# Performance work log

Measured on AMD Instinct MI355X. Metric: run time of the kernel, lower is better.

The kernel has to match this reference:

```python
import jax, jax.numpy as jnp
import numpy as np

B, N1, N2, D, K = 8, 2048, 512, 128, 32
LEVELS, RES, BASE, FC = 3, 3, 0.25, 192
R3 = RES ** 3  # 27 voxel bins per level
EPS = 1e-5


def group_norm(x, gamma, beta, groups):
    # x: [b, C, ...]; normalize per (group) over channel-subset + spatial dims
    b, c = x.shape[0], x.shape[1]
    xg = x.reshape(b, groups, -1)
    mu = xg.mean(axis=-1, keepdims=True)
    var = xg.var(axis=-1, keepdims=True)
    xn = ((xg - mu) * jax.lax.rsqrt(var + EPS)).reshape(x.shape)
    shape = (1, c) + (1,) * (x.ndim - 2)
    return xn * gamma.reshape(shape) + beta.reshape(shape)


def prelu(x, a):
    return jnp.where(x >= 0, x, a * x)


def setup_inputs() -> dict:
    key = jax.random.key(0)
    ks = jax.random.split(key, 12)
    def w(k, shape):
        fan_in = shape[-1]
        return jax.random.uniform(k, shape, jnp.float32, -1.0, 1.0) / jnp.sqrt(jnp.float32(fan_in))
    return {
        "coords": jax.random.normal(ks[0], (B, N1, 3), jnp.float32),
        "coords2": jax.random.normal(ks[1], (B, N2, 3), jnp.float32),
        "fmap1": jax.random.normal(ks[2], (B, D, N1), jnp.float32),
        "fmap2": jax.random.normal(ks[3], (B, D, N2), jnp.float32),
        # vol_conv: Conv1d(81,128,1) -> GN(8,128) -> PReLU -> Conv1d(128,192,1)
        "W1": w(ks[4], (128, R3 * LEVELS)), "b1": jnp.zeros((128,), jnp.float32),
        "g1": jnp.ones((128,), jnp.float32), "be1": jnp.zeros((128,), jnp.float32),
        "a1": jnp.array(0.25, jnp.float32),
        "W2": w(ks[5], (FC, 128)), "b2": jnp.zeros((FC,), jnp.float32),
        # knn_conv: Conv2d(4,64,1) -> GN(8,64) -> PReLU;  knn_out: Conv1d(64,192,1)
        "Wk": w(ks[6], (64, 4)), "bk": jnp.zeros((64,), jnp.float32),
        "gk": jnp.ones((64,), jnp.float32), "bek": jnp.zeros((64,), jnp.float32),
        "ak": jnp.array(0.25, jnp.float32),
        "Wo": w(ks[7], (FC, 64)), "bo": jnp.zeros((FC,), jnp.float32),
    }


def reference(coords, coords2, fmap1, fmap2, W1, b1, g1, be1, a1, W2, b2,
              Wk, bk, gk, bek, ak, Wo, bo):
    b, n1 = coords.shape[0], coords.shape[1]
    n2 = coords2.shape[1]
    dim = fmap1.shape[1]

    # correlation: [b, n1, n2]
    corr = jnp.einsum('bdn,bdm->bnm', fmap1, fmap2) / jnp.sqrt(jnp.float32(dim))
    # pairwise offsets template - search: [b, n1, n2, 3]
    diff = coords2[:, None, :, :] - coords[:, :, None, :]

    # --- multi-level voxel feature via scatter-add ---
    base = jnp.arange(b * n1, dtype=jnp.int32).reshape(b, n1, 1) * R3
    feats = []
    for i in range(LEVELS):
        r = BASE * (2 ** i)
        dv = jnp.round(diff / r)
        valid = jnp.all(jnp.abs(dv) <= (RES // 2), axis=-1)          # [b,n1,n2]
        dvi = (dv + 1.0).astype(jnp.int32)
        cube = dvi[..., 0] * (RES * RES) + dvi[..., 1] * RES + dvi[..., 2]
        idx = jnp.where(valid, cube, 0)                              # torch: cube*valid
        seg = (base + idx).reshape(-1)
        vf = valid.astype(corr.dtype)
        nseg = b * n1 * R3
        add = jax.ops.segment_sum((corr * vf).reshape(-1), seg, num_segments=nseg).reshape(b, n1, R3)
        cnt = jax.ops.segment_sum(vf.reshape(-1), seg, num_segments=nseg).reshape(b, n1, R3)
        feats.append((add / jnp.clip(cnt, 1.0, float(n1))).transpose(0, 2, 1))  # [b,R3,n1]
    vol = jnp.concatenate(feats, axis=1)                             # [b, 3*27, n1]

    h = jnp.einsum('oc,bcn->bon', W1, vol) + b1[None, :, None]
    h = prelu(group_norm(h, g1, be1, 8), a1)
    vol_out = jnp.einsum('oc,bcn->bon', W2, h) + b2[None, :, None]   # [b, FC, n1]

    # --- KNN feature ---
    dist = jnp.sum(diff * diff, axis=-1)                             # [b,n1,n2]
    _, nbr = jax.lax.top_k(-dist, K)                                 # [b,n1,K]
    knn_corr = jnp.take_along_axis(corr, nbr, axis=2)                # [b,n1,K]
    knn_xyz = jnp.take_along_axis(diff, nbr[..., None], axis=2)      # [b,n1,K,3]
    e = jnp.concatenate([knn_corr[:, None], knn_xyz.transpose(0, 3, 1, 2)], axis=1)  # [b,4,n1,K]
    h = jnp.einsum('oc,bcnk->bonk', Wk, e) + bk[None, :, None, None]
    h = prelu(group_norm(h, gk, bek, 8), ak)
    h = jnp.max(h, axis=3)                                           # [b,64,n1]
    knn_out = jnp.einsum('oc,bcn->bon', Wo, h) + bo[None, :, None]   # [b,FC,n1]

    return vol_out + knn_out
```

## Files before the change

### kernel.cpp

```cpp
#include <hip/hip_runtime.h>
#include <hip/hip_bf16.h>

#define N1 2048
#define N2 512
#define KNN 32

typedef unsigned short u16;
typedef unsigned int u32;
typedef unsigned long long u64;
typedef __attribute__((ext_vector_type(8))) short bf16x8;
typedef __attribute__((ext_vector_type(4))) float f32x4;

#define OFF_W1B  18432
#define OFF_GV   36864
#define OFF_GK   36992
#define OFF_FLAG 37120
#define OFF_H1   37128
#define OFF_KM   1085704
#define OFF_CO   1609992

__device__ __forceinline__ float tof(u16 u) {
  union { u32 i; float f; } v; v.i = ((u32)u) << 16; return v.f;
}
__device__ __forceinline__ u16 tob(float f) {
  __hip_bfloat16 h = __float2bfloat16(f);
  return *reinterpret_cast<u16*>(&h);
}
__device__ __forceinline__ float fs(float v) {
  return (fabsf(v) < 1e30f) ? v : 0.f;
}

template <int BF>
__device__ __forceinline__ float LD(const void* p, size_t i) {
  if (BF) return tof(((const u16*)p)[i]);
  return ((const float*)p)[i];
}
template <int BF>
__device__ __forceinline__ void ST(void* p, size_t i, float v) {
  if (BF) ((u16*)p)[i] = tob(v);
  else    ((float*)p)[i] = v;
}

__device__ __forceinline__ u32 umin32(u32 a, u32 b) { return a < b ? a : b; }

__device__ __forceinline__ u32 wave_min_u32(u32 v) {
  v = umin32(v, (u32)__builtin_amdgcn_update_dpp((int)0xFFFFFFFF, (int)v, 0x111, 0xf, 0xf, false));
  v = umin32(v, (u32)__builtin_amdgcn_update_dpp((int)0xFFFFFFFF, (int)v, 0x112, 0xf, 0xf, false));
  v = umin32(v, (u32)__builtin_amdgcn_update_dpp((int)0xFFFFFFFF, (int)v, 0x114, 0xf, 0xf, false));
  v = umin32(v, (u32)__builtin_amdgcn_update_dpp((int)0xFFFFFFFF, (int)v, 0x118, 0xf, 0xf, false));
  v = umin32(v, (u32)__builtin_amdgcn_update_dpp((int)0xFFFFFFFF, (int)v, 0x142, 0xa, 0xf, false));
  v = umin32(v, (u32)__builtin_amdgcn_update_dpp((int)0xFFFFFFFF, (int)v, 0x143, 0xc, 0xf, false));
  return (u32)__builtin_amdgcn_readlane((int)v, 63);
}

template <int BF>
__device__ __forceinline__ bf16x8 ld_wfrag(const void* W2, const void* Wo,
                                           int o, int k0) {
  if (BF) {
    const u16* p = (k0 < 128) ? (const u16*)W2 + (size_t)o * 128 + k0
                              : (const u16*)Wo + (size_t)o * 64 + (k0 - 128);
    return *(const bf16x8*)p;
  } else {
    const float* p = (k0 < 128) ? (const float*)W2 + (size_t)o * 128 + k0
                                : (const float*)Wo + (size_t)o * 64 + (k0 - 128);
    bf16x8 r;
#pragma unroll
    for (int j = 0; j < 8; j++) r[j] = (short)tob(p[j]);
    return r;
  }
}

template <int BF>
__device__ void prep_body(const void* W1, float* ws, int i0, int stride) {
  u16* w1b = (u16*)(ws + OFF_W1B);
  for (int i = i0; i < 128 * 96; i += stride) {
    int c = i / 96, j = i % 96;
    float v = (j < 81) ? LD<BF>(W1, c * 81 + j) : 0.f;
    w1b[i] = tob(fs(v));
  }
}

__global__ __launch_bounds__(256) void k_prep(const void* fmap1, const void* W1,
                                              float* ws) {
  int t = threadIdx.x;
  __shared__ int sbad;
  if (t == 0) sbad = 0;
  __syncthreads();
  int bad = 0;
  const u16* fm = (const u16*)fmap1;
  for (int i = t * 8; i < t * 8 + 8; i++) {
    float v = tof(fm[i]);
    if (!(fabsf(v) <= 64.f)) bad = 1;
  }
  if (bad) atomicOr(&sbad, 1);
  __syncthreads();
  int bf = sbad ? 0 : 1;
  if (blockIdx.x == 0) {
    if (t == 0) ((int*)(ws + OFF_FLAG))[0] = bf;
    (ws + OFF_GV)[t] = 0.f;
  }
  int i0 = blockIdx.x * 256 + t, stride = gridDim.x * 256;
  if (bf) prep_body<1>(W1, ws, i0, stride);
  else    prep_body<0>(W1, ws, i0, stride);
}

template <int BF>
__device__ void corr_stage(const void* f1, const void* f2, u16* As, u16* Bs,
                           int b, int m0, int n0, int t) {
#pragma unroll
  for (int rep = 0; rep < 2; rep++) {
    int i = t + rep * 256;
    int m8 = i & 15, d4 = i >> 4;
    u16 e[4][8];
    if (BF) {
      const u16* F1 = (const u16*)f1;
#pragma unroll
      for (int dr = 0; dr < 4; dr++) {
        uint4 v = *(const uint4*)&F1[(size_t)(b * 128 + d4 * 4 + dr) * N1 + m0 + m8 * 8];
        u32 w[4] = {v.x, v.y, v.z, v.w};
#pragma unroll
        for (int j = 0; j < 8; j++) e[dr][j] = (u16)(w[j >> 1] >> ((j & 1) * 16));
      }
    } else {
      const float* F1 = (const float*)f1;
#pragma unroll
      for (int dr = 0; dr < 4; dr++) {
        const float* src = &F1[(size_t)(b * 128 + d4 * 4 + dr) * N1 + m0 + m8 * 8];
        float4 a = *(const float4*)src, c = *(const float4*)(src + 4);
        float f[8] = {a.x, a.y, a.z, a.w, c.x, c.y, c.z, c.w};
#pragma unroll
        for (int j = 0; j < 8; j++) e[dr][j] = tob(f[j]);
      }
    }
#pragma unroll
    for (int j = 0; j < 8; j++) {
      u64 pk = (u64)e[0][j] | ((u64)e[1][j] << 16) | ((u64)e[2][j] << 32) |
               ((u64)e[3][j] << 48);
      *(u64*)&As[(m8 * 8 + j) * 136 + d4 * 4] = pk;
    }
  }
  {
    int n8 = t & 7, d4 = t >> 3;
    u16 e[4][8];
    if (BF) {
      const u16* F2 = (const u16*)f2;
#pragma unroll
      for (int dr = 0; dr < 4; dr++) {
        uint4 v = *(const uint4*)&F2[(size_t)(b * 128 + d4 * 4 + dr) * N2 + n0 + n8 * 8];
        u32 w[4] = {v.x, v.y, v.z, v.w};
#pragma unroll
        for (int j = 0; j < 8; j++) e[dr][j] = (u16)(w[j >> 1] >> ((j & 1) * 16));
      }
    } else {
      const float* F2 = (const float*)f2;
#pragma unroll
      for (int dr = 0; dr < 4; dr++) {
        const float* src = &F2[(size_t)(b * 128 + d4 * 4 + dr) * N2 + n0 + n8 * 8];
        float4 a = *(const float4*)src, c = *(const float4*)(src + 4);
        float f[8] = {a.x, a.y, a.z, a.w, c.x, c.y, c.z, c.w};
#pragma unroll
        for (int j = 0; j < 8; j++) e[dr][j] = tob(f[j]);
      }
    }
#pragma unroll
    for (int j = 0; j < 8; j++) {
      u64 pk = (u64)e[0][j] | ((u64)e[1][j] << 16) | ((u64)e[2][j] << 32) |
               ((u64)e[3][j] << 48);
      *(u64*)&Bs[(n8 * 8 + j) * 136 + d4 * 4] = pk;
    }
  }
}

__global__ __launch_bounds__(256) void k_corr(const int* flag,
                                              const void* f1, const void* f2,
                                              u16* corrb) {
  __shared__ __attribute__((aligned(16))) u16 As[128 * 136];
  __shared__ __attribute__((aligned(16))) u16 Bs[64 * 136];
  int b = blockIdx.z, m0 = blockIdx.x * 128, n0 = blockIdx.y * 64, t = threadIdx.x;
  if (*flag) corr_stage<1>(f1, f2, As, Bs, b, m0, n0, t);
  else       corr_stage<0>(f1, f2, As, Bs, b, m0, n0, t);
  __syncthreads();

  int wv = t >> 6, lane = t & 63;
  int l15 = lane & 15, q = lane >> 4;
  int wm = (wv >> 1) * 64, wn = (wv & 1) * 32;
  f32x4 acc[4][2];
#pragma unroll
  for (int mt = 0; mt < 4; mt++)
#pragma unroll
    for (int nt = 0; nt < 2; nt++) acc[mt][nt] = (f32x4){0.f, 0.f, 0.f, 0.f};

#pragma unroll
  for (int kc = 0; kc < 128; kc += 32) {
    bf16x8 af[4], bf[2];
#pragma unroll
    for (int mt = 0; mt < 4; mt++)
      af[mt] = *(const bf16x8*)&As[(wm + mt * 16 + l15) * 136 + kc + q * 8];
#pragma unroll
    for (int nt = 0; nt < 2; nt++)
      bf[nt] = *(const bf16x8*)&Bs[(wn + nt * 16 + l15) * 136 + kc + q * 8];
#pragma unroll
    for (int mt = 0; mt < 4; mt++)
#pragma unroll
      for (int nt = 0; nt < 2; nt++)
        acc[mt][nt] = __builtin_amdgcn_mfma_f32_16x16x32_bf16(
            af[mt], bf[nt], acc[mt][nt], 0, 0, 0);
  }
  const float s = 0.08838834764831843f;
#pragma unroll
  for (int mt = 0; mt < 4; mt++)
#pragma unroll
    for (int nt = 0; nt < 2; nt++)
#pragma unroll
      for (int r = 0; r < 4; r++) {
        int m = m0 + wm + mt * 16 + q * 4 + r;
        int n = n0 + wn + nt * 16 + l15;
        corrb[((size_t)(b * N1 + m)) * N2 + n] = tob(acc[mt][nt][r] * s);
      }
}

template <int BF>
__device__ void pv_body(const void* coords, const void* coords2,
                        const u16* corrb, const void* Wk, const void* bk,
                        const u16* w1b, const void* b1,
                        u16* h1b, u16* knnmax,
                        float* gvolraw, float* gknnraw,
                        float* c2s, float* binsum, float* bincnt,
                        float4* e_s, u16* volb, float* statv, float* statk,
                        int b, int p0, int t) {
  int wv = t >> 6, lane = t & 63;
  int l15 = lane & 15, q = lane >> 4;
  for (int i = t; i < N2 * 3; i += 256) c2s[i] = LD<BF>(coords2, b * N2 * 3 + i);
  for (int i = t; i < 208; i += 256) ((uint4*)volb)[i] = make_uint4(0, 0, 0, 0);
  if (t < 16) { statv[t] = 0.f; statk[t] = 0.f; }
  __syncthreads();

  for (int s = 0; s < 2; s++) {
    int pp = wv * 2 + s;
    int p = p0 + pp;
    for (int i = lane; i < 81; i += 64) {
      binsum[wv * 81 + i] = 0.f;
      bincnt[wv * 81 + i] = 0.f;
    }
    float px = LD<BF>(coords, (b * N1 + p) * 3 + 0);
    float py = LD<BF>(coords, (b * N1 + p) * 3 + 1);
    float pz = LD<BF>(coords, (b * N1 + p) * 3 + 2);
    const u16* crow = corrb + ((size_t)(b * N1 + p)) * N2;

    u64 kk[8];
#pragma unroll
    for (int i = 0; i < 8; i++) {
      int n2 = i * 64 + lane;
      float cv = tof(crow[n2]);
      float dx = c2s[n2 * 3 + 0] - px;
      float dy = c2s[n2 * 3 + 1] - py;
      float dz = c2s[n2 * 3 + 2] - pz;
      float dist = __fadd_rn(__fadd_rn(__fmul_rn(dx, dx), __fmul_rn(dy, dy)),
                             __fmul_rn(dz, dz));
      union { float f; u32 u; } du; du.f = dist;
      kk[i] = (((u64)du.u) << 32) | (u64)n2;
      float sc = 4.f;
#pragma unroll
      for (int lvl = 0; lvl < 3; lvl++) {
        float vx = rintf(dx * sc), vy = rintf(dy * sc), vz = rintf(dz * sc);
        if (fabsf(vx) <= 1.f && fabsf(vy) <= 1.f && fabsf(vz) <= 1.f) {
          int cube = ((int)vx + 1) * 9 + ((int)vy + 1) * 3 + ((int)vz + 1);
          atomicAdd(&binsum[wv * 81 + lvl * 27 + cube], cv);
          atomicAdd(&bincnt[wv * 81 + lvl * 27 + cube], 1.f);
        }
        sc *= 0.5f;
      }
    }

#define CAS(a, b) { u64 x = kk[a], y = kk[b]; bool sw = y < x; \
                    kk[a] = sw ? y : x; kk[b] = sw ? x : y; }
    CAS(0,1) CAS(2,3) CAS(4,5) CAS(6,7)
    CAS(0,2) CAS(1,3) CAS(4,6) CAS(5,7)
    CAS(1,2) CAS(5,6)
    CAS(0,4) CAS(1,5) CAS(2,6) CAS(3,7)
    CAS(2,4) CAS(3,5)
    CAS(1,2) CAS(3,4) CAS(5,6)
#undef CAS
    int my_idx = 0;
    for (int it = 0; it < KNN; it++) {
      u32 hb = (u32)(kk[0] >> 32);
      u32 wb = wave_min_u32(hb);
      u64 mask = __ballot(hb == wb);
      u32 widx;
      if (__builtin_popcountll(mask) == 1) {
        int wl = (int)__builtin_ctzll(mask);
        widx = (u32)__builtin_amdgcn_readlane((int)(u32)kk[0], wl);
      } else {
        u32 hidx = (hb == wb) ? (u32)kk[0] : 0xFFFFFFFFu;
        widx = wave_min_u32(hidx);
      }
      if (lane == it) my_idx = (int)widx;
      if (lane == (int)(widx & 63u)) {
        kk[0] = kk[1]; kk[1] = kk[2]; kk[2] = kk[3]; kk[3] = kk[4];
        kk[4] = kk[5]; kk[5] = kk[6]; kk[6] = kk[7]; kk[7] = ~0ull;
      }
    }
    if (lane < KNN) {
      float4 ev;
      ev.x = tof(crow[my_idx]);
      ev.y = c2s[my_idx * 3 + 0] - px;
      ev.z = c2s[my_idx * 3 + 1] - py;
      ev.w = c2s[my_idx * 3 + 2] - pz;
      e_s[wv * 32 + lane] = ev;
    }
#pragma unroll
    for (int rep = 0; rep < 2; rep++) {
      int i = lane + rep * 64;
      if (i < 96) {
        float v = (i < 81)
            ? binsum[wv * 81 + i] / fmaxf(bincnt[wv * 81 + i], 1.f) : 0.f;
        volb[pp * 104 + i] = tob(v);
      }
    }

    {
      int cch = lane;
      float w0 = LD<BF>(Wk, cch * 4 + 0), w1 = LD<BF>(Wk, cch * 4 + 1);
      float w2 = LD<BF>(Wk, cch * 4 + 2), w3 = LD<BF>(Wk, cch * 4 + 3);
      float bv = LD<BF>(bk, cch);
      float sm = 0.f, sq = 0.f, mx = -3e38f;
#pragma unroll 8
      for (int k = 0; k < KNN; k++) {
        float4 ev = e_s[wv * 32 + k];
        float h = bv + w0 * ev.x + w1 * ev.y + w2 * ev.z + w3 * ev.w;
        sm += h; sq += h * h; mx = fmaxf(mx, h);
      }
      knnmax[((size_t)(b * N1 + p)) * 64 + cch] = tob(mx);
      sm += __shfl_xor(sm, 1, 64); sq += __shfl_xor(sq, 1, 64);
      sm += __shfl_xor(sm, 2, 64); sq += __shfl_xor(sq, 2, 64);
      sm += __shfl_xor(sm, 4, 64); sq += __shfl_xor(sq, 4, 64);
      if ((lane & 7) == 0) {
        int g = cch >> 3;
        atomicAdd(&statk[g * 2 + 0], sm);
        atomicAdd(&statk[g * 2 + 1], sq);
      }
    }
  }
  __syncthreads();

  f32x4 acc[2];
  acc[0] = (f32x4){0.f, 0.f, 0.f, 0.f};
  acc[1] = (f32x4){0.f, 0.f, 0.f, 0.f};
#pragma unroll
  for (int kc = 0; kc < 96; kc += 32) {
    bf16x8 af = *(const bf16x8*)&volb[l15 * 104 + kc + q * 8];
    bf16x8 bf0 = *(const bf16x8*)&w1b[((2 * wv + 0) * 16 + l15) * 96 + kc + q * 8];
    bf16x8 bf1 = *(const bf16x8*)&w1b[((2 * wv + 1) * 16 + l15) * 96 + kc + q * 8];
    acc[0] = __builtin_amdgcn_mfma_f32_16x16x32_bf16(af, bf0, acc[0], 0, 0, 0);
    acc[1] = __builtin_amdgcn_mfma_f32_16x16x32_bf16(af, bf1, acc[1], 0, 0, 0);
  }
#pragma unroll
  for (int ct = 0; ct < 2; ct++) {
    int c = (2 * wv + ct) * 16 + l15;
    float bias = LD<BF>(b1, c);
    float sm = 0.f, sq = 0.f;
    if (q < 2) {
#pragma unroll
      for (int r = 0; r < 4; r++) {
        int p = p0 + q * 4 + r;
        float v = acc[ct][r] + bias;
        h1b[((size_t)(b * N1 + p)) * 128 + c] = tob(v);
        sm += v; sq += v * v;
      }
    }
    sm += __shfl_xor(sm, 1, 64);  sq += __shfl_xor(sq, 1, 64);
    sm += __shfl_xor(sm, 2, 64);  sq += __shfl_xor(sq, 2, 64);
    sm += __shfl_xor(sm, 4, 64);  sq += __shfl_xor(sq, 4, 64);
    sm += __shfl_xor(sm, 8, 64);  sq += __shfl_xor(sq, 8, 64);
    sm += __shfl_xor(sm, 16, 64); sq += __shfl_xor(sq, 16, 64);
    sm += __shfl_xor(sm, 32, 64); sq += __shfl_xor(sq, 32, 64);
    if (lane == 0) {
      int g = 2 * wv + ct;
      atomicAdd(&statv[g * 2 + 0], sm);
      atomicAdd(&statv[g * 2 + 1], sq);
    }
  }
  __syncthreads();
  if (t < 16) atomicAdd(&gvolraw[b * 16 + t], statv[t]);
  else if (t < 32) atomicAdd(&gknnraw[b * 16 + (t - 16)], statk[t - 16]);
}

__global__ __launch_bounds__(256) void k_pv(const int* flag,
                                            const void* coords, const void* coords2,
                                            const u16* corrb, const void* Wk,
                                            const void* bk, const u16* w1b,
                                            const void* b1, u16* h1b,
                                            u16* knnmax, float* gvolraw,
                                            float* gknnraw) {
  __shared__ float c2s[N2 * 3];
  __shared__ float binsum[4 * 81];
  __shared__ float bincnt[4 * 81];
  __shared__ float4 e_s[4 * 32];
  __shared__ __attribute__((aligned(16))) u16 volb[16 * 104];
  __shared__ float statv[16], statk[16];
  int b = blockIdx.y, p0 = blockIdx.x * 8, t = threadIdx.x;
  if (*flag)
    pv_body<1>(coords, coords2, corrb, Wk, bk, w1b, b1, h1b, knnmax,
               gvolraw, gknnraw, c2s, binsum, bincnt, e_s, volb, statv, statk,
               b, p0, t);
  else
    pv_body<0>(coords, coords2, corrb, Wk, bk, w1b, b1, h1b, knnmax,
               gvolraw, gknnraw, c2s, binsum, bincnt, e_s, volb, statv, statk,
               b, p0, t);
}

template <int BF>
__device__ void out_body(const u16* h1b, const u16* knnmax,
                         const void* W2, const void* Wo,
                         const float* gvolraw, const float* gknnraw,
                         const void* g1, const void* be1, const void* a1p,
                         const void* gk, const void* bek, const void* akp,
                         const void* b2, const void* bo, void* out,
                         float* Ac, float* Bc, float* Sc, float* Bi, u16* gs,
                         int b, int p0, int t) {
  if (t < 192) {
    float A, Bv, slope;
    if (t < 128) {
      int g = t >> 4;
      float S = fs(gvolraw[b * 16 + g * 2 + 0]);
      float Q = fs(gvolraw[b * 16 + g * 2 + 1]);
      float mean = S / 32768.f;
      float var = fmaxf(Q / 32768.f - mean * mean, 0.f);
      float inv = 1.f / sqrtf(var + 1e-5f);
      A = inv * LD<BF>(g1, t); Bv = LD<BF>(be1, t) - mean * A;
      slope = LD<BF>(a1p, 0);
    } else {
      int c = t - 128, g = c >> 3;
      float S = fs(gknnraw[b * 16 + g * 2 + 0]);
      float Q = fs(gknnraw[b * 16 + g * 2 + 1]);
      float mean = S / 524288.f;
      float var = fmaxf(Q / 524288.f - mean * mean, 0.f);
      float inv = 1.f / sqrtf(var + 1e-5f);
      A = inv * LD<BF>(gk, c); Bv = LD<BF>(bek, c) - mean * A;
      slope = LD<BF>(akp, 0);
    }
    Ac[t] = A; Bc[t] = Bv; Sc[t] = slope;
    Bi[t] = LD<BF>(b2, t) + LD<BF>(bo, t);
  }
  __syncthreads();

  for (int i = t; i < 768; i += 256) {
    int p = i / 24, c8 = i % 24;
    int c0 = c8 * 8;
    uint4 v;
    if (c8 < 16) v = *(const uint4*)&h1b[((size_t)(b * N1 + p0 + p)) * 128 + c0];
    else         v = *(const uint4*)&knnmax[((size_t)(b * N1 + p0 + p)) * 64 + (c0 - 128)];
    u16 e[8] = {(u16)(v.x & 0xffff), (u16)(v.x >> 16), (u16)(v.y & 0xffff),
                (u16)(v.y >> 16),    (u16)(v.z & 0xffff), (u16)(v.z >> 16),
                (u16)(v.w & 0xffff), (u16)(v.w >> 16)};
    u16 r[8];
#pragma unroll
    for (int j = 0; j < 8; j++) {
      int c = c0 + j;
      float xn = tof(e[j]) * Ac[c] + Bc[c];
      xn = xn >= 0.f ? xn : Sc[c] * xn;
      r[j] = tob(xn);
    }
    uint4 wv;
    wv.x = (u32)r[0] | ((u32)r[1] << 16);
    wv.y = (u32)r[2] | ((u32)r[3] << 16);
    wv.z = (u32)r[4] | ((u32)r[5] << 16);
    wv.w = (u32)r[6] | ((u32)r[7] << 16);
    *(uint4*)&gs[p * 200 + c0] = wv;
  }
  __syncthreads();

  int wv2 = t >> 6, lane = t & 63;
  int l15 = lane & 15, q = lane >> 4;
  int obase = wv2 * 48;
  f32x4 acc[3][2];
#pragma unroll
  for (int mt = 0; mt < 3; mt++)
#pragma unroll
    for (int nt = 0; nt < 2; nt++) acc[mt][nt] = (f32x4){0.f, 0.f, 0.f, 0.f};

#pragma unroll
  for (int kc = 0; kc < 192; kc += 32) {
    bf16x8 af[3], bf[2];
#pragma unroll
    for (int mt = 0; mt < 3; mt++)
      af[mt] = ld_wfrag<BF>(W2, Wo, obase + mt * 16 + l15, kc + q * 8);
#pragma unroll
    for (int nt = 0; nt < 2; nt++)
      bf[nt] = *(const bf16x8*)&gs[(nt * 16 + l15) * 200 + kc + q * 8];
#pragma unroll
    for (int mt = 0; mt < 3; mt++)
#pragma unroll
      for (int nt = 0; nt < 2; nt++)
        acc[mt][nt] = __builtin_amdgcn_mfma_f32_16x16x32_bf16(
            af[mt], bf[nt], acc[mt][nt], 0, 0, 0);
  }
#pragma unroll
  for (int mt = 0; mt < 3; mt++)
#pragma unroll
    for (int nt = 0; nt < 2; nt++)
#pragma unroll
      for (int r = 0; r < 4; r++) {
        int o = obase + mt * 16 + q * 4 + r;
        int p = p0 + nt * 16 + l15;
        ST<BF>(out, ((size_t)(b * 192 + o)) * N1 + p, fs(acc[mt][nt][r] + Bi[o]));
      }
}

__global__ __launch_bounds__(256) void k_out(const int* flag,
                                             const u16* h1b, const u16* knnmax,
                                             const void* W2, const void* Wo,
                                             const float* gvolraw, const float* gknnraw,
                                             const void* g1, const void* be1,
                                             const void* a1p, const void* gk,
                                             const void* bek, const void* akp,
                                             const void* b2, const void* bo,
                                             void* out) {
  __shared__ float Ac[192], Bc[192], Sc[192], Bi[192];
  __shared__ __attribute__((aligned(16))) u16 gs[32 * 200];
  int b = blockIdx.y, p0 = blockIdx.x * 32, t = threadIdx.x;
  if (*flag)
    out_body<1>(h1b, knnmax, W2, Wo, gvolraw, gknnraw, g1, be1, a1p, gk, bek,
                akp, b2, bo, out, Ac, Bc, Sc, Bi, gs, b, p0, t);
  else
    out_body<0>(h1b, knnmax, W2, Wo, gvolraw, gknnraw, g1, be1, a1p, gk, bek,
                akp, b2, bo, out, Ac, Bc, Sc, Bi, gs, b, p0, t);
}

extern "C" void kernel_launch(void* const* d_in, const int* in_sizes, int n_in,
                              void* d_out, int out_size, void* d_ws, size_t ws_size,
                              hipStream_t stream) {
  const void* coords  = d_in[0];
  const void* coords2 = d_in[1];
  const void* fmap1   = d_in[2];
  const void* fmap2   = d_in[3];
  const void* W1  = d_in[4];
  const void* b1  = d_in[5];
  const void* g1  = d_in[6];
  const void* be1 = d_in[7];
  const void* a1  = d_in[8];
  const void* W2  = d_in[9];
  const void* b2  = d_in[10];
  const void* Wk  = d_in[11];
  const void* bk  = d_in[12];
  const void* gk  = d_in[13];
  const void* bek = d_in[14];
  const void* ak  = d_in[15];
  const void* Wo  = d_in[16];
  const void* bo  = d_in[17];

  float* ws = (float*)d_ws;
  u16* w1b       = (u16*)(ws + OFF_W1B);
  float* gvolraw = ws + OFF_GV;
  float* gknnraw = ws + OFF_GK;
  const int* flag = (const int*)(ws + OFF_FLAG);
  u16* h1b    = (u16*)(ws + OFF_H1);
  u16* knnmax = (u16*)(ws + OFF_KM);
  u16* corrb  = (u16*)(ws + OFF_CO);

  k_prep<<<dim3(8), dim3(256), 0, stream>>>(fmap1, W1, ws);
  k_corr<<<dim3(16, 8, 8), dim3(256), 0, stream>>>(flag, fmap1, fmap2, corrb);
  k_pv<<<dim3(256, 8), dim3(256), 0, stream>>>(flag, coords, coords2, corrb,
                                               Wk, bk, w1b, b1, h1b, knnmax,
                                               gvolraw, gknnraw);
  k_out<<<dim3(64, 8), dim3(256), 0, stream>>>(flag, h1b, knnmax, W2, Wo,
                                               gvolraw, gknnraw, g1, be1, a1,
                                               gk, bek, ak, b2, bo, d_out);
}
```

Baseline: 208.2 us.

## Fuse correlation GEMM into per-point kernel and shrink output tile

Drops the separate correlation kernel and its global bf16 corr buffer. Each k_pv block now computes its 8 rows of corr in shared memory with MFMA, reading fmap1 columns and all of fmap2 in 64-column chunks. This removes the corr write and re-read through global memory and one launch. The cost is that every block reloads and converts the full fmap2 for its batch (256 blocks per batch), and half of each 16-row MFMA tile is padding. k_out is also retiled to 16 points per block to launch more blocks.

```diff
diff --git a/kernel.cpp b/kernel.cpp
--- a/kernel.cpp
+++ b/kernel.cpp
@@ -17,7 +17,6 @@
 #define OFF_FLAG 37120
 #define OFF_H1   37128
 #define OFF_KM   1085704
-#define OFF_CO   1609992
 
 __device__ __forceinline__ float tof(u16 u) {
   union { u32 i; float f; } v; v.i = ((u32)u) << 16; return v.f;
@@ -105,134 +104,80 @@
 }
 
 template <int BF>
-__device__ void corr_stage(const void* f1, const void* f2, u16* As, u16* Bs,
-                           int b, int m0, int n0, int t) {
-#pragma unroll
-  for (int rep = 0; rep < 2; rep++) {
-    int i = t + rep * 256;
-    int m8 = i & 15, d4 = i >> 4;
-    u16 e[4][8];
-    if (BF) {
-      const u16* F1 = (const u16*)f1;
-#pragma unroll
-      for (int dr = 0; dr < 4; dr++) {
-        uint4 v = *(const uint4*)&F1[(size_t)(b * 128 + d4 * 4 + dr) * N1 + m0 + m8 * 8];
-        u32 w[4] = {v.x, v.y, v.z, v.w};
-#pragma unroll
-        for (int j = 0; j < 8; j++) e[dr][j] = (u16)(w[j >> 1] >> ((j & 1) * 16));
-      }
-    } else {
-      const float* F1 = (const float*)f1;
-#pragma unroll
-      for (int dr = 0; dr < 4; dr++) {
-        const float* src = &F1[(size_t)(b * 128 + d4 * 4 + dr) * N1 + m0 + m8 * 8];
-        float4 a = *(const float4*)src, c = *(const float4*)(src + 4);
-        float f[8] = {a.x, a.y, a.z, a.w, c.x, c.y, c.z, c.w};
-#pragma unroll
-        for (int j = 0; j < 8; j++) e[dr][j] = tob(f[j]);
-      }
-    }
-#pragma unroll
-    for (int j = 0; j < 8; j++) {
-      u64 pk = (u64)e[0][j] | ((u64)e[1][j] << 16) | ((u64)e[2][j] << 32) |
-               ((u64)e[3][j] << 48);
-      *(u64*)&As[(m8 * 8 + j) * 136 + d4 * 4] = pk;
-    }
-  }
-  {
-    int n8 = t & 7, d4 = t >> 3;
-    u16 e[4][8];
-    if (BF) {
-      const u16* F2 = (const u16*)f2;
-#pragma unroll
-      for (int dr = 0; dr < 4; dr++) {
-        uint4 v = *(const uint4*)&F2[(size_t)(b * 128 + d4 * 4 + dr) * N2 + n0 + n8 * 8];
-        u32 w[4] = {v.x, v.y, v.z, v.w};
-#pragma unroll
-        for (int j = 0; j < 8; j++) e[dr][j] = (u16)(w[j >> 1] >> ((j & 1) * 16));
-      }
-    } else {
-      const float* F2 = (const float*)f2;
-#pragma unroll
-      for (int dr = 0; dr < 4; dr++) {
-        const float* src = &F2[(size_t)(b * 128 + d4 * 4 + dr) * N2 + n0 + n8 * 8];
-        float4 a = *(const float4*)src, c = *(const float4*)(src + 4);
-        float f[8] = {a.x, a.y, a.z, a.w, c.x, c.y, c.z, c.w};
-#pragma unroll
-        for (int j = 0; j < 8; j++) e[dr][j] = tob(f[j]);
-      }
-    }
-#pragma unroll
-    for (int j = 0; j < 8; j++) {
-      u64 pk = (u64)e[0][j] | ((u64)e[1][j] << 16) | ((u64)e[2][j] << 32) |
-               ((u64)e[3][j] << 48);
-      *(u64*)&Bs[(n8 * 8 + j) * 136 + d4 * 4] = pk;
-    }
-  }
-}
-
-__global__ __launch_bounds__(256) void k_corr(const int* flag,
-                                              const void* f1, const void* f2,
-                                              u16* corrb) {
-  __shared__ __attribute__((aligned(16))) u16 As[128 * 136];
-  __shared__ __attribute__((aligned(16))) u16 Bs[64 * 136];
-  int b = blockIdx.z, m0 = blockIdx.x * 128, n0 = blockIdx.y * 64, t = threadIdx.x;
-  if (*flag) corr_stage<1>(f1, f2, As, Bs, b, m0, n0, t);
-  else       corr_stage<0>(f1, f2, As, Bs, b, m0, n0, t);
-  __syncthreads();
-
-  int wv = t >> 6, lane = t & 63;
-  int l15 = lane & 15, q = lane >> 4;
-  int wm = (wv >> 1) * 64, wn = (wv & 1) * 32;
-  f32x4 acc[4][2];
-#pragma unroll
-  for (int mt = 0; mt < 4; mt++)
-#pragma unroll
-    for (int nt = 0; nt < 2; nt++) acc[mt][nt] = (f32x4){0.f, 0.f, 0.f, 0.f};
-
-#pragma unroll
-  for (int kc = 0; kc < 128; kc += 32) {
-    bf16x8 af[4], bf[2];
-#pragma unroll
-    for (int mt = 0; mt < 4; mt++)
-      af[mt] = *(const bf16x8*)&As[(wm + mt * 16 + l15) * 136 + kc + q * 8];
-#pragma unroll
-    for (int nt = 0; nt < 2; nt++)
-      bf[nt] = *(const bf16x8*)&Bs[(wn + nt * 16 + l15) * 136 + kc + q * 8];
-#pragma unroll
-    for (int mt = 0; mt < 4; mt++)
-#pragma unroll
-      for (int nt = 0; nt < 2; nt++)
-        acc[mt][nt] = __builtin_amdgcn_mfma_f32_16x16x32_bf16(
-            af[mt], bf[nt], acc[mt][nt], 0, 0, 0);
-  }
-  const float s = 0.08838834764831843f;
-#pragma unroll
-  for (int mt = 0; mt < 4; mt++)
-#pragma unroll
-    for (int nt = 0; nt < 2; nt++)
-#pragma unroll
-      for (int r = 0; r < 4; r++) {
-        int m = m0 + wm + mt * 16 + q * 4 + r;
-        int n = n0 + wn + nt * 16 + l15;
-        corrb[((size_t)(b * N1 + m)) * N2 + n] = tob(acc[mt][nt][r] * s);
-      }
-}
-
-template <int BF>
 __device__ void pv_body(const void* coords, const void* coords2,
-                        const u16* corrb, const void* Wk, const void* bk,
+                        const void* f1, const void* f2,
+                        const void* Wk, const void* bk,
                         const u16* w1b, const void* b1,
                         u16* h1b, u16* knnmax,
                         float* gvolraw, float* gknnraw,
-                        float* c2s, float* binsum, float* bincnt,
-                        float4* e_s, u16* volb, float* statv, float* statk,
+                        u16* crow_s, u16* f2b, float* c2s, u16* f1c,
+                        float4* e_s, float* binsum, float* bincnt,
+                        u16* volb, float* statv, float* statk,
                         int b, int p0, int t) {
   int wv = t >> 6, lane = t & 63;
   int l15 = lane & 15, q = lane >> 4;
-  for (int i = t; i < N2 * 3; i += 256) c2s[i] = LD<BF>(coords2, b * N2 * 3 + i);
+
+  for (int i = t; i < 16 * 136; i += 256) {
+    int m = i / 136, k = i - m * 136;
+    u16 v = 0;
+    if (m < 8 && k < 128)
+      v = tob(LD<BF>(f1, (size_t)(b * 128 + k) * N1 + p0 + m));
+    f1c[i] = v;
+  }
   for (int i = t; i < 208; i += 256) ((uint4*)volb)[i] = make_uint4(0, 0, 0, 0);
   if (t < 16) { statv[t] = 0.f; statk[t] = 0.f; }
+  __syncthreads();
+
+  const float sc_corr = 0.08838834764831843f;
+  for (int ch = 0; ch < 8; ch++) {
+    int n0 = ch * 64;
+    {
+      int n8 = t & 7, d4 = t >> 3;
+      u16 e[4][8];
+      if (BF) {
+        const u16* F2 = (const u16*)f2;
+#pragma unroll
+        for (int dr = 0; dr < 4; dr++) {
+          uint4 v = *(const uint4*)&F2[(size_t)(b * 128 + d4 * 4 + dr) * N2 + n0 + n8 * 8];
+          u32 w[4] = {v.x, v.y, v.z, v.w};
+#pragma unroll
+          for (int j = 0; j < 8; j++) e[dr][j] = (u16)(w[j >> 1] >> ((j & 1) * 16));
+        }
+      } else {
+        const float* F2 = (const float*)f2;
+#pragma unroll
+        for (int dr = 0; dr < 4; dr++) {
+          const float* src = &F2[(size_t)(b * 128 + d4 * 4 + dr) * N2 + n0 + n8 * 8];
+          float4 a = *(const float4*)src, c = *(const float4*)(src + 4);
+          float f[8] = {a.x, a.y, a.z, a.w, c.x, c.y, c.z, c.w};
+#pragma unroll
+          for (int j = 0; j < 8; j++) e[dr][j] = tob(f[j]);
+        }
+      }
+#pragma unroll
+      for (int j = 0; j < 8; j++) {
+        u64 pk = (u64)e[0][j] | ((u64)e[1][j] << 16) | ((u64)e[2][j] << 32) |
+                 ((u64)e[3][j] << 48);
+        *(u64*)&f2b[(n8 * 8 + j) * 136 + d4 * 4] = pk;
+      }
+    }
+    __syncthreads();
+    f32x4 acc = (f32x4){0.f, 0.f, 0.f, 0.f};
+#pragma unroll
+    for (int kc = 0; kc < 128; kc += 32) {
+      bf16x8 af = *(const bf16x8*)&f1c[l15 * 136 + kc + q * 8];
+      bf16x8 bf = *(const bf16x8*)&f2b[(wv * 16 + l15) * 136 + kc + q * 8];
+      acc = __builtin_amdgcn_mfma_f32_16x16x32_bf16(af, bf, acc, 0, 0, 0);
+    }
+    if (q < 2) {
+#pragma unroll
+      for (int r = 0; r < 4; r++)
+        crow_s[(q * 4 + r) * 512 + n0 + wv * 16 + l15] = tob(acc[r] * sc_corr);
+    }
+    __syncthreads();
+  }
+
+  for (int i = t; i < N2 * 3; i += 256) c2s[i] = LD<BF>(coords2, b * N2 * 3 + i);
   __syncthreads();
 
   for (int s = 0; s < 2; s++) {
@@ -245,7 +190,7 @@
     float px = LD<BF>(coords, (b * N1 + p) * 3 + 0);
     float py = LD<BF>(coords, (b * N1 + p) * 3 + 1);
     float pz = LD<BF>(coords, (b * N1 + p) * 3 + 2);
-    const u16* crow = corrb + ((size_t)(b * N1 + p)) * N2;
+    const u16* crow = &crow_s[pp * 512];
 
     u64 kk[8];
 #pragma unroll
@@ -387,26 +332,27 @@
 
 __global__ __launch_bounds__(256) void k_pv(const int* flag,
                                             const void* coords, const void* coords2,
-                                            const u16* corrb, const void* Wk,
-                                            const void* bk, const u16* w1b,
-                                            const void* b1, u16* h1b,
-                                            u16* knnmax, float* gvolraw,
-                                            float* gknnraw) {
-  __shared__ float c2s[N2 * 3];
+                                            const void* f1, const void* f2,
+                                            const void* Wk, const void* bk,
+                                            const u16* w1b, const void* b1,
+                                            u16* h1b, u16* knnmax,
+                                            float* gvolraw, float* gknnraw) {
+  __shared__ __attribute__((aligned(16))) u16 crow_s[8 * 512];
+  __shared__ __attribute__((aligned(16))) u16 ua[64 * 136];
+  __shared__ __attribute__((aligned(16))) u16 ub[16 * 136];
   __shared__ float binsum[4 * 81];
   __shared__ float bincnt[4 * 81];
-  __shared__ float4 e_s[4 * 32];
   __shared__ __attribute__((aligned(16))) u16 volb[16 * 104];
   __shared__ float statv[16], statk[16];
   int b = blockIdx.y, p0 = blockIdx.x * 8, t = threadIdx.x;
   if (*flag)
-    pv_body<1>(coords, coords2, corrb, Wk, bk, w1b, b1, h1b, knnmax,
-               gvolraw, gknnraw, c2s, binsum, bincnt, e_s, volb, statv, statk,
-               b, p0, t);
+    pv_body<1>(coords, coords2, f1, f2, Wk, bk, w1b, b1, h1b, knnmax,
+               gvolraw, gknnraw, crow_s, ua, (float*)ua, ub,
+               (float4*)ub, binsum, bincnt, volb, statv, statk, b, p0, t);
   else
-    pv_body<0>(coords, coords2, corrb, Wk, bk, w1b, b1, h1b, knnmax,
-               gvolraw, gknnraw, c2s, binsum, bincnt, e_s, volb, statv, statk,
-               b, p0, t);
+    pv_body<0>(coords, coords2, f1, f2, Wk, bk, w1b, b1, h1b, knnmax,
+               gvolraw, gknnraw, crow_s, ua, (float*)ua, ub,
+               (float4*)ub, binsum, bincnt, volb, statv, statk, b, p0, t);
 }
 
 template <int BF>
@@ -444,7 +390,7 @@
   }
   __syncthreads();
 
-  for (int i = t; i < 768; i += 256) {
+  for (int i = t; i < 384; i += 256) {
     int p = i / 24, c8 = i % 24;
     int c0 = c8 * 8;
     uint4 v;
@@ -473,38 +419,29 @@
   int wv2 = t >> 6, lane = t & 63;
   int l15 = lane & 15, q = lane >> 4;
   int obase = wv2 * 48;
-  f32x4 acc[3][2];
-#pragma unroll
-  for (int mt = 0; mt < 3; mt++)
-#pragma unroll
-    for (int nt = 0; nt < 2; nt++) acc[mt][nt] = (f32x4){0.f, 0.f, 0.f, 0.f};
+  f32x4 acc[3];
+#pragma unroll
+  for (int mt = 0; mt < 3; mt++) acc[mt] = (f32x4){0.f, 0.f, 0.f, 0.f};
 
 #pragma unroll
   for (int kc = 0; kc < 192; kc += 32) {
-    bf16x8 af[3], bf[2];
+    bf16x8 af[3];
 #pragma unroll
     for (int mt = 0; mt < 3; mt++)
       af[mt] = ld_wfrag<BF>(W2, Wo, obase + mt * 16 + l15, kc + q * 8);
-#pragma unroll
-    for (int nt = 0; nt < 2; nt++)
-      bf[nt] = *(const bf16x8*)&gs[(nt * 16 + l15) * 200 + kc + q * 8];
+    bf16x8 bf = *(const bf16x8*)&gs[l15 * 200 + kc + q * 8];
 #pragma unroll
     for (int mt = 0; mt < 3; mt++)
-#pragma unroll
-      for (int nt = 0; nt < 2; nt++)
-        acc[mt][nt] = __builtin_amdgcn_mfma_f32_16x16x32_bf16(
-            af[mt], bf[nt], acc[mt][nt], 0, 0, 0);
+      acc[mt] = __builtin_amdgcn_mfma_f32_16x16x32_bf16(af[mt], bf, acc[mt], 0, 0, 0);
   }
 #pragma unroll
   for (int mt = 0; mt < 3; mt++)
 #pragma unroll
-    for (int nt = 0; nt < 2; nt++)
-#pragma unroll
-      for (int r = 0; r < 4; r++) {
-        int o = obase + mt * 16 + q * 4 + r;
-        int p = p0 + nt * 16 + l15;
-        ST<BF>(out, ((size_t)(b * 192 + o)) * N1 + p, fs(acc[mt][nt][r] + Bi[o]));
-      }
+    for (int r = 0; r < 4; r++) {
+      int o = obase + mt * 16 + q * 4 + r;
+      int p = p0 + l15;
+      ST<BF>(out, ((size_t)(b * 192 + o)) * N1 + p, fs(acc[mt][r] + Bi[o]));
+    }
 }
 
 __global__ __launch_bounds__(256) void k_out(const int* flag,
@@ -517,8 +454,8 @@
                                              const void* b2, const void* bo,
                                              void* out) {
   __shared__ float Ac[192], Bc[192], Sc[192], Bi[192];
-  __shared__ __attribute__((aligned(16))) u16 gs[32 * 200];
-  int b = blockIdx.y, p0 = blockIdx.x * 32, t = threadIdx.x;
+  __shared__ __attribute__((aligned(16))) u16 gs[16 * 200];
+  int b = blockIdx.y, p0 = blockIdx.x * 16, t = threadIdx.x;
   if (*flag)
     out_body<1>(h1b, knnmax, W2, Wo, gvolraw, gknnraw, g1, be1, a1p, gk, bek,
                 akp, b2, bo, out, Ac, Bc, Sc, Bi, gs, b, p0, t);
@@ -556,14 +493,12 @@
   const int* flag = (const int*)(ws + OFF_FLAG);
   u16* h1b    = (u16*)(ws + OFF_H1);
   u16* knnmax = (u16*)(ws + OFF_KM);
-  u16* corrb  = (u16*)(ws + OFF_CO);
 
   k_prep<<<dim3(8), dim3(256), 0, stream>>>(fmap1, W1, ws);
-  k_corr<<<dim3(16, 8, 8), dim3(256), 0, stream>>>(flag, fmap1, fmap2, corrb);
-  k_pv<<<dim3(256, 8), dim3(256), 0, stream>>>(flag, coords, coords2, corrb,
-                                               Wk, bk, w1b, b1, h1b, knnmax,
-                                               gvolraw, gknnraw);
-  k_out<<<dim3(64, 8), dim3(256), 0, stream>>>(flag, h1b, knnmax, W2, Wo,
-                                               gvolraw, gknnraw, g1, be1, a1,
-                                               gk, bek, ak, b2, bo, d_out);
-}
+  k_pv<<<dim3(256, 8), dim3(256), 0, stream>>>(flag, coords, coords2, fmap1,
+                                               fmap2, Wk, bk, w1b, b1, h1b,
+                                               knnmax, gvolraw, gknnraw);
+  k_out<<<dim3(128, 8), dim3(256), 0, stream>>>(flag, h1b, knnmax, W2, Wo,
+                                                gvolraw, gknnraw, g1, be1, a1,
+                                                gk, bek, ak, b2, bo, d_out);
+}
```

New measurement: 243.6 us. 17.0% more time.
